# Performance work log

Measured on AMD Instinct MI355X. Metric: run time of the kernel, lower is better.

The kernel has to match this reference:

```python
import jax, jax.numpy as jnp
import numpy as np

C_Q = 256
C_K = 256
C_V = 256
C_HID = 32
N_HEADS = 8
HD = C_HID * N_HEADS  # 256


def setup_inputs() -> dict:
    key = jax.random.key(0)
    ks = jax.random.split(key, 12)
    B, Q, K = 1, 2048, 2048
    s = 0.02
    return {
        "q_x": jax.random.normal(ks[0], (B, Q, C_Q), jnp.float32),
        "kv_x": jax.random.normal(ks[1], (B, K, C_K), jnp.float32),
        "bias_mask": jax.random.normal(ks[2], (B, 1, 1, K), jnp.float32),
        "bias_pair": jax.random.normal(ks[3], (B, N_HEADS, Q, K), jnp.float32),
        "Wq": jax.random.normal(ks[4], (C_Q, HD), jnp.float32) * s,
        "Wk": jax.random.normal(ks[5], (C_K, HD), jnp.float32) * s,
        "Wv": jax.random.normal(ks[6], (C_V, HD), jnp.float32) * s,
        "Wo": jax.random.normal(ks[7], (HD, C_Q), jnp.float32) * s,
        "bo": jnp.zeros((C_Q,), jnp.float32),
        "Wg": jax.random.normal(ks[8], (C_Q, HD), jnp.float32) * s,
        "bg": jnp.ones((HD,), jnp.float32),
    }


def reference(q_x, kv_x, bias_mask, bias_pair, Wq, Wk, Wv, Wo, bo, Wg, bg):
    B, Qn, _ = q_x.shape
    Kn = kv_x.shape[1]
    # QKV projections -> [B, H, L, c_hidden]
    q = (q_x @ Wq).reshape(B, Qn, N_HEADS, C_HID).transpose(0, 2, 1, 3)
    k = (kv_x @ Wk).reshape(B, Kn, N_HEADS, C_HID).transpose(0, 2, 1, 3)
    v = (kv_x @ Wv).reshape(B, Kn, N_HEADS, C_HID).transpose(0, 2, 1, 3)
    q = q / jnp.sqrt(jnp.asarray(C_HID, q.dtype))
    # scores [B, H, Q, K] with additive biases
    a = jnp.einsum("bhqc,bhkc->bhqk", q, k) + bias_mask + bias_pair
    a = jax.nn.softmax(a, axis=-1)
    o = jnp.einsum("bhqk,bhkc->bhqc", a, v)  # [B, H, Q, c_hidden]
    o = o.transpose(0, 2, 1, 3)              # [B, Q, H, c_hidden]
    # sigmoid gate from query data
    g = jax.nn.sigmoid(q_x @ Wg + bg).reshape(B, Qn, N_HEADS, C_HID)
    o = o * g
    o = o.reshape(B, Qn, HD)
    return o @ Wo + bo
```

## Files before the change

kernel.cpp:

```cpp
#include <hip/hip_runtime.h>
#include <hip/hip_bf16.h>
#include <stdint.h>

#define N_TOK 2048
#define C_IN 256
#define HEADS 8
#define DH 32
#define HDIM 256
#define LOG2E 1.4426950408889634f

typedef __attribute__((ext_vector_type(8))) short short8;
typedef __attribute__((ext_vector_type(4))) float float4_t;

__device__ __forceinline__ short f2b(float f) {
    unsigned u = __builtin_bit_cast(unsigned, f);
    unsigned r = (u + 0x7FFFu + ((u >> 16) & 1u)) >> 16;
    return (short)(r & 0xFFFFu);
}

__global__ void prep_x(const float* __restrict__ qx, const float* __restrict__ kvx,
                       short* __restrict__ Xq, short* __restrict__ Xkv) {
    int idx = blockIdx.x * blockDim.x + threadIdx.x;
    int base = idx * 8;
    const int NX = N_TOK * C_IN;
    const float* src; short* dst; int off;
    if (base < NX) { src = qx;  dst = Xq;  off = base; }
    else           { src = kvx; dst = Xkv; off = base - NX; }
    float4_t a = *(const float4_t*)(src + off);
    float4_t b = *(const float4_t*)(src + off + 4);
    short8 o;
    o[0] = f2b(a[0]); o[1] = f2b(a[1]); o[2] = f2b(a[2]); o[3] = f2b(a[3]);
    o[4] = f2b(b[0]); o[5] = f2b(b[1]); o[6] = f2b(b[2]); o[7] = f2b(b[3]);
    *(short8*)(dst + off) = o;
}

__global__ void prep_w(const float* __restrict__ Wq, const float* __restrict__ Wk,
                       const float* __restrict__ Wv, const float* __restrict__ Wg,
                       const float* __restrict__ Wo,
                       short* __restrict__ Wtq, short* __restrict__ Wtk,
                       short* __restrict__ Wtv, short* __restrict__ Wtg,
                       short* __restrict__ Wto) {
    int wi = blockIdx.y;
    int j = blockIdx.x;
    int c = threadIdx.x;
    const float* W; short* Wt;
    switch (wi) {
        case 0: W = Wq; Wt = Wtq; break;
        case 1: W = Wk; Wt = Wtk; break;
        case 2: W = Wv; Wt = Wtv; break;
        case 3: W = Wg; Wt = Wtg; break;
        default: W = Wo; Wt = Wto; break;
    }
    Wt[j * 256 + c] = f2b(W[c * 256 + j]);
}

__global__ void proj_nh(const short* __restrict__ Xq, const short* __restrict__ Xkv,
                        const short* __restrict__ Wtq, const short* __restrict__ Wtk,
                        const short* __restrict__ Wtg, const float* __restrict__ bg,
                        short* __restrict__ qh, short* __restrict__ kh,
                        float* __restrict__ gsig) {
    int tid = threadIdx.x, wave = tid >> 6, lane = tid & 63, g16 = lane >> 4, li = lane & 15;
    int mode = blockIdx.z;
    const short* X  = (mode == 1) ? Xkv : Xq;
    const short* Wt = (mode == 0) ? Wtq : (mode == 1 ? Wtk : Wtg);
    int n0 = blockIdx.x * 64 + wave * 16;
    int c0 = blockIdx.y * 64;
    float4_t acc[4];
#pragma unroll
    for (int j = 0; j < 4; j++) acc[j] = (float4_t){0.f, 0.f, 0.f, 0.f};
    for (int k0 = 0; k0 < C_IN; k0 += 32) {
        short8 a = *(const short8*)(X + (n0 + li) * C_IN + k0 + g16 * 8);
#pragma unroll
        for (int j = 0; j < 4; j++) {
            short8 b = *(const short8*)(Wt + (c0 + j * 16 + li) * C_IN + k0 + g16 * 8);
            acc[j] = __builtin_amdgcn_mfma_f32_16x16x32_bf16(a, b, acc[j], 0, 0, 0);
        }
    }
#pragma unroll
    for (int j = 0; j < 4; j++) {
#pragma unroll
        for (int r = 0; r < 4; r++) {
            int n = n0 + g16 * 4 + r;
            int col = c0 + j * 16 + li;
            float v = acc[j][r];
            if (mode == 0) {
                qh[(col >> 5) * (N_TOK * DH) + n * DH + (col & 31)] =
                    f2b(v * 0.17677669529663687f);
            } else if (mode == 1) {
                kh[(col >> 5) * (N_TOK * DH) + n * DH + (col & 31)] = f2b(v);
            } else {
                float x = v + bg[col];
                gsig[n * HDIM + col] = 1.f / (1.f + __expf(-x));
            }
        }
    }
}

__global__ void proj_hn(const short* __restrict__ Xkv, const short* __restrict__ Wtv,
                        short* __restrict__ vt) {
    int tid = threadIdx.x, wave = tid >> 6, lane = tid & 63, g16 = lane >> 4, li = lane & 15;
    int hd0 = blockIdx.x * 64 + wave * 16;
    int n0 = blockIdx.y * 64;
    float4_t acc[4];
#pragma unroll
    for (int j = 0; j < 4; j++) acc[j] = (float4_t){0.f, 0.f, 0.f, 0.f};
    for (int k0 = 0; k0 < C_IN; k0 += 32) {
        short8 a = *(const short8*)(Wtv + (hd0 + li) * C_IN + k0 + g16 * 8);
#pragma unroll
        for (int j = 0; j < 4; j++) {
            short8 b = *(const short8*)(Xkv + (n0 + j * 16 + li) * C_IN + k0 + g16 * 8);
            acc[j] = __builtin_amdgcn_mfma_f32_16x16x32_bf16(a, b, acc[j], 0, 0, 0);
        }
    }
#pragma unroll
    for (int j = 0; j < 4; j++) {
#pragma unroll
        for (int r = 0; r < 4; r++) {
            int hd = hd0 + g16 * 4 + r;
            int n = n0 + j * 16 + li;
            vt[hd * N_TOK + n] = f2b(acc[j][r]);
        }
    }
}

__global__ void attn(const short* __restrict__ qh, const short* __restrict__ kh,
                     const short* __restrict__ vt, const float* __restrict__ bias_mask,
                     const float* __restrict__ bias_pair, const float* __restrict__ gsig,
                     short* __restrict__ OG) {
    __shared__ short plds[4][16][72];
    int tid = threadIdx.x, wave = tid >> 6, lane = tid & 63, g16 = lane >> 4, li = lane & 15;
    int h = blockIdx.y, qb = blockIdx.x;
    int qbase = qb * 64 + wave * 16;
    const short* qp = qh + h * (N_TOK * DH);
    const short* kp = kh + h * (N_TOK * DH);
    const short* vp = vt + h * (DH * N_TOK);
    short8 qa = *(const short8*)(qp + (qbase + li) * DH + g16 * 8);
    const float* bpp = bias_pair + (size_t)(h * N_TOK + qbase) * N_TOK;
    float m[4], l[4];
    float4_t o0 = {0.f, 0.f, 0.f, 0.f}, o1 = {0.f, 0.f, 0.f, 0.f};
#pragma unroll
    for (int r = 0; r < 4; r++) { m[r] = -1e30f; l[r] = 0.f; }
    const float4_t z4 = {0.f, 0.f, 0.f, 0.f};

    for (int kb = 0; kb < N_TOK; kb += 64) {
        float4_t s[4];
#pragma unroll
        for (int t = 0; t < 4; t++) {
            short8 kf = *(const short8*)(kp + (kb + t * 16 + li) * DH + g16 * 8);
            s[t] = __builtin_amdgcn_mfma_f32_16x16x32_bf16(qa, kf, z4, 0, 0, 0);
        }
        float bm[4];
#pragma unroll
        for (int t = 0; t < 4; t++) bm[t] = bias_mask[kb + t * 16 + li];
        float bp[4][4];
#pragma unroll
        for (int t = 0; t < 4; t++)
#pragma unroll
            for (int r = 0; r < 4; r++)
                bp[t][r] = bpp[(g16 * 4 + r) * N_TOK + kb + t * 16 + li];
        float sc[4][4];
#pragma unroll
        for (int t = 0; t < 4; t++)
#pragma unroll
            for (int r = 0; r < 4; r++) sc[t][r] = s[t][r] + bm[t] + bp[t][r];

#pragma unroll
        for (int r = 0; r < 4; r++) {
            float mx = fmaxf(fmaxf(sc[0][r], sc[1][r]), fmaxf(sc[2][r], sc[3][r]));
#pragma unroll
            for (int off = 1; off < 16; off <<= 1) mx = fmaxf(mx, __shfl_xor(mx, off));
            float mn = fmaxf(m[r], mx);
            float sscale = exp2f((m[r] - mn) * LOG2E);
            float su = 0.f;
#pragma unroll
            for (int t = 0; t < 4; t++) {
                float p = exp2f((sc[t][r] - mn) * LOG2E);
                sc[t][r] = p;
                su += p;
            }
#pragma unroll
            for (int off = 1; off < 16; off <<= 1) su += __shfl_xor(su, off);
            l[r] = l[r] * sscale + su;
            m[r] = mn;
            o0[r] *= sscale;
            o1[r] *= sscale;
        }

#pragma unroll
        for (int t = 0; t < 4; t++)
#pragma unroll
            for (int r = 0; r < 4; r++)
                plds[wave][g16 * 4 + r][t * 16 + li] = f2b(sc[t][r]);
        short8 pa0 = *(const short8*)&plds[wave][li][g16 * 8];
        short8 pa1 = *(const short8*)&plds[wave][li][32 + g16 * 8];

        short8 v00 = *(const short8*)(vp + li * N_TOK + kb + g16 * 8);
        short8 v01 = *(const short8*)(vp + li * N_TOK + kb + 32 + g16 * 8);
        short8 v10 = *(const short8*)(vp + (16 + li) * N_TOK + kb + g16 * 8);
        short8 v11 = *(const short8*)(vp + (16 + li) * N_TOK + kb + 32 + g16 * 8);
        o0 = __builtin_amdgcn_mfma_f32_16x16x32_bf16(pa0, v00, o0, 0, 0, 0);
        o0 = __builtin_amdgcn_mfma_f32_16x16x32_bf16(pa1, v01, o0, 0, 0, 0);
        o1 = __builtin_amdgcn_mfma_f32_16x16x32_bf16(pa0, v10, o1, 0, 0, 0);
        o1 = __builtin_amdgcn_mfma_f32_16x16x32_bf16(pa1, v11, o1, 0, 0, 0);
    }

#pragma unroll
    for (int r = 0; r < 4; r++) {
        float inv = 1.f / l[r];
        int n = qbase + g16 * 4 + r;
        int col0 = h * DH + li;
        int col1 = h * DH + 16 + li;
        OG[n * HDIM + col0] = f2b(o0[r] * inv * gsig[n * HDIM + col0]);
        OG[n * HDIM + col1] = f2b(o1[r] * inv * gsig[n * HDIM + col1]);
    }
}

__global__ void outproj(const short* __restrict__ OG, const short* __restrict__ Wto,
                        const float* __restrict__ bo, float* __restrict__ out) {
    int tid = threadIdx.x, wave = tid >> 6, lane = tid & 63, g16 = lane >> 4, li = lane & 15;
    int n0 = blockIdx.x * 64 + wave * 16;
    int c0 = blockIdx.y * 64;
    float4_t acc[4];
#pragma unroll
    for (int j = 0; j < 4; j++) acc[j] = (float4_t){0.f, 0.f, 0.f, 0.f};
    for (int k0 = 0; k0 < HDIM; k0 += 32) {
        short8 a = *(const short8*)(OG + (n0 + li) * HDIM + k0 + g16 * 8);
#pragma unroll
        for (int j = 0; j < 4; j++) {
            short8 b = *(const short8*)(Wto + (c0 + j * 16 + li) * HDIM + k0 + g16 * 8);
            acc[j] = __builtin_amdgcn_mfma_f32_16x16x32_bf16(a, b, acc[j], 0, 0, 0);
        }
    }
#pragma unroll
    for (int j = 0; j < 4; j++) {
#pragma unroll
        for (int r = 0; r < 4; r++) {
            int n = n0 + g16 * 4 + r;
            int col = c0 + j * 16 + li;
            out[n * C_IN + col] = acc[j][r] + bo[col];
        }
    }
}

extern "C" void kernel_launch(void* const* d_in, const int* in_sizes, int n_in,
                              void* d_out, int out_size, void* d_ws, size_t ws_size,
                              hipStream_t stream) {
    const float* q_x       = (const float*)d_in[0];
    const float* kv_x      = (const float*)d_in[1];
    const float* bias_mask = (const float*)d_in[2];
    const float* bias_pair = (const float*)d_in[3];
    const float* Wq        = (const float*)d_in[4];
    const float* Wk        = (const float*)d_in[5];
    const float* Wv        = (const float*)d_in[6];
    const float* Wo        = (const float*)d_in[7];
    const float* bo        = (const float*)d_in[8];
    const float* Wg        = (const float*)d_in[9];
    const float* bg        = (const float*)d_in[10];
    float* out = (float*)d_out;
    char* ws = (char*)d_ws;

    short* Xq   = (short*)(ws);
    short* Xkv  = (short*)(ws + (1u << 20));
    short* Wtq  = (short*)(ws + (2u << 20));
    short* Wtk  = Wtq + 65536;
    short* Wtv  = Wtk + 65536;
    short* Wtg  = Wtv + 65536;
    short* Wto  = Wtg + 65536;
    short* qhb  = (short*)(ws + (3u << 20));
    short* khb  = (short*)(ws + (4u << 20));
    short* vtb  = (short*)(ws + (5u << 20));
    float* gsig = (float*)(ws + (6u << 20));
    short* OG   = (short*)(ws + (8u << 20));

    hipLaunchKernelGGL(prep_x, dim3(512), dim3(256), 0, stream, q_x, kv_x, Xq, Xkv);
    hipLaunchKernelGGL(prep_w, dim3(256, 5), dim3(256), 0, stream,
                       Wq, Wk, Wv, Wg, Wo, Wtq, Wtk, Wtv, Wtg, Wto);
    hipLaunchKernelGGL(proj_nh, dim3(32, 4, 3), dim3(256), 0, stream,
                       Xq, Xkv, Wtq, Wtk, Wtg, bg, qhb, khb, gsig);
    hipLaunchKernelGGL(proj_hn, dim3(4, 32), dim3(256), 0, stream, Xkv, Wtv, vtb);
    hipLaunchKernelGGL(attn, dim3(32, 8), dim3(256), 0, stream,
                       qhb, khb, vtb, bias_mask, bias_pair, gsig, OG);
    hipLaunchKernelGGL(outproj, dim3(32, 4), dim3(256), 0, stream, OG, Wto, bo, out);
}
```

Before: 287.2 us.

## Split attention keys across waves, merge kernels, shrink projection tiles

Attention now gives each 16-query tile one 512-thread block. The eight waves each process a 256-key slice, and the partial max, sum and output are combined through shared memory. This is a split-K flash decoding scheme meant to raise parallelism and the number of blocks in flight. The prep kernels are merged into one, with a shared-memory tiled weight transpose. The q/k/g/v projections are merged into one launch with smaller 16x16 tiles per wave, and outproj uses smaller tiles too. Hardware exp2 intrinsics replace exp2f. Each wave does less compute per block, and the final reduction adds shared memory use and a sync.

```diff
diff --git a/kernel.cpp b/kernel.cpp
--- a/kernel.cpp
+++ b/kernel.cpp
@@ -18,131 +18,125 @@
     return (short)(r & 0xFFFFu);
 }
 
-__global__ void prep_x(const float* __restrict__ qx, const float* __restrict__ kvx,
-                       short* __restrict__ Xq, short* __restrict__ Xkv) {
-    int idx = blockIdx.x * blockDim.x + threadIdx.x;
-    int base = idx * 8;
-    const int NX = N_TOK * C_IN;
-    const float* src; short* dst; int off;
-    if (base < NX) { src = qx;  dst = Xq;  off = base; }
-    else           { src = kvx; dst = Xkv; off = base - NX; }
-    float4_t a = *(const float4_t*)(src + off);
-    float4_t b = *(const float4_t*)(src + off + 4);
-    short8 o;
-    o[0] = f2b(a[0]); o[1] = f2b(a[1]); o[2] = f2b(a[2]); o[3] = f2b(a[3]);
-    o[4] = f2b(b[0]); o[5] = f2b(b[1]); o[6] = f2b(b[2]); o[7] = f2b(b[3]);
-    *(short8*)(dst + off) = o;
-}
-
-__global__ void prep_w(const float* __restrict__ Wq, const float* __restrict__ Wk,
-                       const float* __restrict__ Wv, const float* __restrict__ Wg,
-                       const float* __restrict__ Wo,
-                       short* __restrict__ Wtq, short* __restrict__ Wtk,
-                       short* __restrict__ Wtv, short* __restrict__ Wtg,
-                       short* __restrict__ Wto) {
-    int wi = blockIdx.y;
-    int j = blockIdx.x;
-    int c = threadIdx.x;
-    const float* W; short* Wt;
-    switch (wi) {
-        case 0: W = Wq; Wt = Wtq; break;
-        case 1: W = Wk; Wt = Wtk; break;
-        case 2: W = Wv; Wt = Wtv; break;
-        case 3: W = Wg; Wt = Wtg; break;
-        default: W = Wo; Wt = Wto; break;
-    }
-    Wt[j * 256 + c] = f2b(W[c * 256 + j]);
-}
-
-__global__ void proj_nh(const short* __restrict__ Xq, const short* __restrict__ Xkv,
-                        const short* __restrict__ Wtq, const short* __restrict__ Wtk,
-                        const short* __restrict__ Wtg, const float* __restrict__ bg,
-                        short* __restrict__ qh, short* __restrict__ kh,
-                        float* __restrict__ gsig) {
+__global__ void prep(const float* __restrict__ qx, const float* __restrict__ kvx,
+                     const float* __restrict__ Wq, const float* __restrict__ Wk,
+                     const float* __restrict__ Wv, const float* __restrict__ Wg,
+                     const float* __restrict__ Wo,
+                     short* __restrict__ Xq, short* __restrict__ Xkv,
+                     short* __restrict__ Wtbase) {
+    __shared__ short S[64][72];
+    int bid = blockIdx.x, tid = threadIdx.x;
+    if (bid < 512) {
+        int base = (bid * 256 + tid) * 8;
+        const int NX = N_TOK * C_IN;
+        const float* src; short* dst; int off;
+        if (base < NX) { src = qx;  dst = Xq;  off = base; }
+        else           { src = kvx; dst = Xkv; off = base - NX; }
+        float4_t a = *(const float4_t*)(src + off);
+        float4_t b = *(const float4_t*)(src + off + 4);
+        short8 o;
+        o[0] = f2b(a[0]); o[1] = f2b(a[1]); o[2] = f2b(a[2]); o[3] = f2b(a[3]);
+        o[4] = f2b(b[0]); o[5] = f2b(b[1]); o[6] = f2b(b[2]); o[7] = f2b(b[3]);
+        *(short8*)(dst + off) = o;
+        return;
+    }
+    int b = bid - 512;
+    int wi = b >> 4, t = b & 15;
+    const float* W = (wi == 0) ? Wq : (wi == 1) ? Wk : (wi == 2) ? Wv : (wi == 3) ? Wg : Wo;
+    short* Wt = Wtbase + wi * 65536;
+    int r0 = (t >> 2) * 64, c0 = (t & 3) * 64;
+    int tr = tid >> 4, tc = tid & 15;
+#pragma unroll
+    for (int i = 0; i < 4; i++) {
+        int rr = tr + i * 16;
+        float4_t v = *(const float4_t*)(W + (r0 + rr) * 256 + c0 + tc * 4);
+        S[tc * 4 + 0][rr] = f2b(v[0]);
+        S[tc * 4 + 1][rr] = f2b(v[1]);
+        S[tc * 4 + 2][rr] = f2b(v[2]);
+        S[tc * 4 + 3][rr] = f2b(v[3]);
+    }
+    __syncthreads();
+    int cr = tid >> 3, co = (tid & 7) * 8;
+#pragma unroll
+    for (int i = 0; i < 2; i++) {
+        int c = cr + i * 32;
+        short8 v = *(const short8*)&S[c][co];
+        *(short8*)(Wt + (c0 + c) * 256 + r0 + co) = v;
+    }
+}
+
+__global__ void proj(const short* __restrict__ Xq, const short* __restrict__ Xkv,
+                     const short* __restrict__ Wtbase, const float* __restrict__ bg,
+                     short* __restrict__ qh, short* __restrict__ kh,
+                     short* __restrict__ vt, float* __restrict__ gsig) {
+    int mode = blockIdx.y;
     int tid = threadIdx.x, wave = tid >> 6, lane = tid & 63, g16 = lane >> 4, li = lane & 15;
-    int mode = blockIdx.z;
-    const short* X  = (mode == 1) ? Xkv : Xq;
-    const short* Wt = (mode == 0) ? Wtq : (mode == 1 ? Wtk : Wtg);
-    int n0 = blockIdx.x * 64 + wave * 16;
-    int c0 = blockIdx.y * 64;
-    float4_t acc[4];
-#pragma unroll
-    for (int j = 0; j < 4; j++) acc[j] = (float4_t){0.f, 0.f, 0.f, 0.f};
-    for (int k0 = 0; k0 < C_IN; k0 += 32) {
-        short8 a = *(const short8*)(X + (n0 + li) * C_IN + k0 + g16 * 8);
-#pragma unroll
-        for (int j = 0; j < 4; j++) {
-            short8 b = *(const short8*)(Wt + (c0 + j * 16 + li) * C_IN + k0 + g16 * 8);
-            acc[j] = __builtin_amdgcn_mfma_f32_16x16x32_bf16(a, b, acc[j], 0, 0, 0);
-        }
-    }
-#pragma unroll
-    for (int j = 0; j < 4; j++) {
-#pragma unroll
-        for (int r = 0; r < 4; r++) {
-            int n = n0 + g16 * 4 + r;
-            int col = c0 + j * 16 + li;
-            float v = acc[j][r];
-            if (mode == 0) {
-                qh[(col >> 5) * (N_TOK * DH) + n * DH + (col & 31)] =
-                    f2b(v * 0.17677669529663687f);
-            } else if (mode == 1) {
-                kh[(col >> 5) * (N_TOK * DH) + n * DH + (col & 31)] = f2b(v);
-            } else {
-                float x = v + bg[col];
-                gsig[n * HDIM + col] = 1.f / (1.f + __expf(-x));
-            }
-        }
-    }
-}
-
-__global__ void proj_hn(const short* __restrict__ Xkv, const short* __restrict__ Wtv,
-                        short* __restrict__ vt) {
+    const short* A;
+    const short* B;
+    int n0, c0;
+    if (mode < 3) {
+        A = (mode == 1) ? Xkv : Xq;
+        B = Wtbase + (mode == 0 ? 0 : (mode == 1 ? 1 : 3)) * 65536;
+        n0 = (blockIdx.x >> 2) * 16;
+        c0 = ((blockIdx.x & 3) * 4 + wave) * 16;
+    } else {
+        A = Wtbase + 2 * 65536;
+        B = Xkv;
+        n0 = (blockIdx.x >> 5) * 16;
+        c0 = ((blockIdx.x & 31) * 4 + wave) * 16;
+    }
+    float4_t acc = (float4_t){0.f, 0.f, 0.f, 0.f};
+    for (int k0 = 0; k0 < 256; k0 += 32) {
+        short8 a = *(const short8*)(A + (n0 + li) * 256 + k0 + g16 * 8);
+        short8 bfr = *(const short8*)(B + (c0 + li) * 256 + k0 + g16 * 8);
+        acc = __builtin_amdgcn_mfma_f32_16x16x32_bf16(a, bfr, acc, 0, 0, 0);
+    }
+#pragma unroll
+    for (int r = 0; r < 4; r++) {
+        int row = n0 + g16 * 4 + r;
+        int col = c0 + li;
+        float v = acc[r];
+        if (mode == 0) {
+            qh[(col >> 5) * (N_TOK * DH) + row * DH + (col & 31)] =
+                f2b(v * 0.17677669529663687f);
+        } else if (mode == 1) {
+            kh[(col >> 5) * (N_TOK * DH) + row * DH + (col & 31)] = f2b(v);
+        } else if (mode == 2) {
+            float x = v + bg[col];
+            float e = __builtin_amdgcn_exp2f(-x * LOG2E);
+            gsig[row * HDIM + col] = 1.f / (1.f + e);
+        } else {
+            vt[row * N_TOK + col] = f2b(v);
+        }
+    }
+}
+
+__global__ void __launch_bounds__(512, 4)
+attn(const short* __restrict__ qh, const short* __restrict__ kh,
+     const short* __restrict__ vt, const float* __restrict__ bias_mask,
+     const float* __restrict__ bias_pair, const float* __restrict__ gsig,
+     short* __restrict__ OG) {
+    __shared__ short plds[8][16][72];
+    __shared__ float po[8][16][33];
+    __shared__ float pm[8][16];
+    __shared__ float pl[8][16];
     int tid = threadIdx.x, wave = tid >> 6, lane = tid & 63, g16 = lane >> 4, li = lane & 15;
-    int hd0 = blockIdx.x * 64 + wave * 16;
-    int n0 = blockIdx.y * 64;
-    float4_t acc[4];
-#pragma unroll
-    for (int j = 0; j < 4; j++) acc[j] = (float4_t){0.f, 0.f, 0.f, 0.f};
-    for (int k0 = 0; k0 < C_IN; k0 += 32) {
-        short8 a = *(const short8*)(Wtv + (hd0 + li) * C_IN + k0 + g16 * 8);
-#pragma unroll
-        for (int j = 0; j < 4; j++) {
-            short8 b = *(const short8*)(Xkv + (n0 + j * 16 + li) * C_IN + k0 + g16 * 8);
-            acc[j] = __builtin_amdgcn_mfma_f32_16x16x32_bf16(a, b, acc[j], 0, 0, 0);
-        }
-    }
-#pragma unroll
-    for (int j = 0; j < 4; j++) {
-#pragma unroll
-        for (int r = 0; r < 4; r++) {
-            int hd = hd0 + g16 * 4 + r;
-            int n = n0 + j * 16 + li;
-            vt[hd * N_TOK + n] = f2b(acc[j][r]);
-        }
-    }
-}
-
-__global__ void attn(const short* __restrict__ qh, const short* __restrict__ kh,
-                     const short* __restrict__ vt, const float* __restrict__ bias_mask,
-                     const float* __restrict__ bias_pair, const float* __restrict__ gsig,
-                     short* __restrict__ OG) {
-    __shared__ short plds[4][16][72];
-    int tid = threadIdx.x, wave = tid >> 6, lane = tid & 63, g16 = lane >> 4, li = lane & 15;
-    int h = blockIdx.y, qb = blockIdx.x;
-    int qbase = qb * 64 + wave * 16;
+    int h = blockIdx.y, qt = blockIdx.x;
+    int qbase = qt * 16;
     const short* qp = qh + h * (N_TOK * DH);
     const short* kp = kh + h * (N_TOK * DH);
     const short* vp = vt + h * (DH * N_TOK);
     short8 qa = *(const short8*)(qp + (qbase + li) * DH + g16 * 8);
-    const float* bpp = bias_pair + (size_t)(h * N_TOK + qbase) * N_TOK;
+    const float* bpp = bias_pair + ((size_t)h * N_TOK + qbase) * N_TOK;
     float m[4], l[4];
     float4_t o0 = {0.f, 0.f, 0.f, 0.f}, o1 = {0.f, 0.f, 0.f, 0.f};
 #pragma unroll
     for (int r = 0; r < 4; r++) { m[r] = -1e30f; l[r] = 0.f; }
     const float4_t z4 = {0.f, 0.f, 0.f, 0.f};
-
-    for (int kb = 0; kb < N_TOK; kb += 64) {
+    int kbeg = wave * 256;
+
+#pragma unroll 1
+    for (int kb = kbeg; kb < kbeg + 256; kb += 64) {
         float4_t s[4];
 #pragma unroll
         for (int t = 0; t < 4; t++) {
@@ -152,17 +146,12 @@
         float bm[4];
 #pragma unroll
         for (int t = 0; t < 4; t++) bm[t] = bias_mask[kb + t * 16 + li];
-        float bp[4][4];
+        float sc[4][4];
 #pragma unroll
         for (int t = 0; t < 4; t++)
 #pragma unroll
             for (int r = 0; r < 4; r++)
-                bp[t][r] = bpp[(g16 * 4 + r) * N_TOK + kb + t * 16 + li];
-        float sc[4][4];
-#pragma unroll
-        for (int t = 0; t < 4; t++)
-#pragma unroll
-            for (int r = 0; r < 4; r++) sc[t][r] = s[t][r] + bm[t] + bp[t][r];
+                sc[t][r] = s[t][r] + bm[t] + bpp[(g16 * 4 + r) * N_TOK + kb + t * 16 + li];
 
 #pragma unroll
         for (int r = 0; r < 4; r++) {
@@ -170,11 +159,11 @@
 #pragma unroll
             for (int off = 1; off < 16; off <<= 1) mx = fmaxf(mx, __shfl_xor(mx, off));
             float mn = fmaxf(m[r], mx);
-            float sscale = exp2f((m[r] - mn) * LOG2E);
+            float sscale = __builtin_amdgcn_exp2f((m[r] - mn) * LOG2E);
             float su = 0.f;
 #pragma unroll
             for (int t = 0; t < 4; t++) {
-                float p = exp2f((sc[t][r] - mn) * LOG2E);
+                float p = __builtin_amdgcn_exp2f((sc[t][r] - mn) * LOG2E);
                 sc[t][r] = p;
                 su += p;
             }
@@ -206,39 +195,51 @@
 
 #pragma unroll
     for (int r = 0; r < 4; r++) {
-        float inv = 1.f / l[r];
-        int n = qbase + g16 * 4 + r;
-        int col0 = h * DH + li;
-        int col1 = h * DH + 16 + li;
-        OG[n * HDIM + col0] = f2b(o0[r] * inv * gsig[n * HDIM + col0]);
-        OG[n * HDIM + col1] = f2b(o1[r] * inv * gsig[n * HDIM + col1]);
-    }
-}
-
-__global__ void outproj(const short* __restrict__ OG, const short* __restrict__ Wto,
+        po[wave][g16 * 4 + r][li] = o0[r];
+        po[wave][g16 * 4 + r][16 + li] = o1[r];
+    }
+    if (li == 0) {
+#pragma unroll
+        for (int r = 0; r < 4; r++) {
+            pm[wave][g16 * 4 + r] = m[r];
+            pl[wave][g16 * 4 + r] = l[r];
+        }
+    }
+    __syncthreads();
+
+    int row = tid >> 5, d = tid & 31;
+    float M = -1e30f;
+#pragma unroll
+    for (int w = 0; w < 8; w++) M = fmaxf(M, pm[w][row]);
+    float L = 0.f, acc = 0.f;
+#pragma unroll
+    for (int w = 0; w < 8; w++) {
+        float wt = __builtin_amdgcn_exp2f((pm[w][row] - M) * LOG2E);
+        L += pl[w][row] * wt;
+        acc += po[w][row][d] * wt;
+    }
+    int n = qbase + row;
+    int col = h * DH + d;
+    OG[n * HDIM + col] = f2b(acc / L * gsig[n * HDIM + col]);
+}
+
+__global__ void outproj(const short* __restrict__ OG, const short* __restrict__ Wtbase,
                         const float* __restrict__ bo, float* __restrict__ out) {
     int tid = threadIdx.x, wave = tid >> 6, lane = tid & 63, g16 = lane >> 4, li = lane & 15;
-    int n0 = blockIdx.x * 64 + wave * 16;
-    int c0 = blockIdx.y * 64;
-    float4_t acc[4];
-#pragma unroll
-    for (int j = 0; j < 4; j++) acc[j] = (float4_t){0.f, 0.f, 0.f, 0.f};
+    const short* Wto = Wtbase + 4 * 65536;
+    int n0 = (blockIdx.x >> 2) * 16;
+    int c0 = ((blockIdx.x & 3) * 4 + wave) * 16;
+    float4_t acc = (float4_t){0.f, 0.f, 0.f, 0.f};
     for (int k0 = 0; k0 < HDIM; k0 += 32) {
         short8 a = *(const short8*)(OG + (n0 + li) * HDIM + k0 + g16 * 8);
-#pragma unroll
-        for (int j = 0; j < 4; j++) {
-            short8 b = *(const short8*)(Wto + (c0 + j * 16 + li) * HDIM + k0 + g16 * 8);
-            acc[j] = __builtin_amdgcn_mfma_f32_16x16x32_bf16(a, b, acc[j], 0, 0, 0);
-        }
-    }
-#pragma unroll
-    for (int j = 0; j < 4; j++) {
-#pragma unroll
-        for (int r = 0; r < 4; r++) {
-            int n = n0 + g16 * 4 + r;
-            int col = c0 + j * 16 + li;
-            out[n * C_IN + col] = acc[j][r] + bo[col];
-        }
+        short8 b = *(const short8*)(Wto + (c0 + li) * HDIM + k0 + g16 * 8);
+        acc = __builtin_amdgcn_mfma_f32_16x16x32_bf16(a, b, acc, 0, 0, 0);
+    }
+#pragma unroll
+    for (int r = 0; r < 4; r++) {
+        int n = n0 + g16 * 4 + r;
+        int col = c0 + li;
+        out[n * C_IN + col] = acc[r] + bo[col];
     }
 }
 
@@ -259,26 +260,20 @@
     float* out = (float*)d_out;
     char* ws = (char*)d_ws;
 
-    short* Xq   = (short*)(ws);
-    short* Xkv  = (short*)(ws + (1u << 20));
-    short* Wtq  = (short*)(ws + (2u << 20));
-    short* Wtk  = Wtq + 65536;
-    short* Wtv  = Wtk + 65536;
-    short* Wtg  = Wtv + 65536;
-    short* Wto  = Wtg + 65536;
-    short* qhb  = (short*)(ws + (3u << 20));
-    short* khb  = (short*)(ws + (4u << 20));
-    short* vtb  = (short*)(ws + (5u << 20));
-    float* gsig = (float*)(ws + (6u << 20));
-    short* OG   = (short*)(ws + (8u << 20));
-
-    hipLaunchKernelGGL(prep_x, dim3(512), dim3(256), 0, stream, q_x, kv_x, Xq, Xkv);
-    hipLaunchKernelGGL(prep_w, dim3(256, 5), dim3(256), 0, stream,
-                       Wq, Wk, Wv, Wg, Wo, Wtq, Wtk, Wtv, Wtg, Wto);
-    hipLaunchKernelGGL(proj_nh, dim3(32, 4, 3), dim3(256), 0, stream,
-                       Xq, Xkv, Wtq, Wtk, Wtg, bg, qhb, khb, gsig);
-    hipLaunchKernelGGL(proj_hn, dim3(4, 32), dim3(256), 0, stream, Xkv, Wtv, vtb);
-    hipLaunchKernelGGL(attn, dim3(32, 8), dim3(256), 0, stream,
+    short* Xq     = (short*)(ws);
+    short* Xkv    = (short*)(ws + (1u << 20));
+    short* Wtbase = (short*)(ws + (2u << 20));
+    short* qhb    = (short*)(ws + (3u << 20));
+    short* khb    = (short*)(ws + (4u << 20));
+    short* vtb    = (short*)(ws + (5u << 20));
+    float* gsig   = (float*)(ws + (6u << 20));
+    short* OG     = (short*)(ws + (8u << 20));
+
+    hipLaunchKernelGGL(prep, dim3(592), dim3(256), 0, stream,
+                       q_x, kv_x, Wq, Wk, Wv, Wg, Wo, Xq, Xkv, Wtbase);
+    hipLaunchKernelGGL(proj, dim3(512, 4), dim3(256), 0, stream,
+                       Xq, Xkv, Wtbase, bg, qhb, khb, vtb, gsig);
+    hipLaunchKernelGGL(attn, dim3(128, 8), dim3(512), 0, stream,
                        qhb, khb, vtb, bias_mask, bias_pair, gsig, OG);
-    hipLaunchKernelGGL(outproj, dim3(32, 4), dim3(256), 0, stream, OG, Wto, bo, out);
-}
+    hipLaunchKernelGGL(outproj, dim3(512), dim3(256), 0, stream, OG, Wtbase, bo, out);
+}
```

After: 247.2 us. 13.9% less time.
